# Kernel optimization log

Measured on AMD Instinct MI355X. Metric: run time of the kernel, lower is better.

## Reference

```python
import jax, jax.numpy as jnp
import numpy as np

CLIP_MIN = 0.0
CLIP_MAX = 1.0
B, T, F, E, CD = 64, 48, 128, 64, 32


def setup_inputs() -> dict:
    key = jax.random.key(0)
    ks = jax.random.split(key, 8)
    return {
        "input_x": jax.random.uniform(ks[0], (B, T, F), dtype=jnp.float32),
        "mask": jax.random.randint(ks[1], (B, T, F), 0, 2, dtype=jnp.int32),
        "embed0": jax.random.normal(ks[2], (F, E), dtype=jnp.float32) * 0.1,
        "embed1": jax.random.normal(ks[3], (F, E), dtype=jnp.float32) * 0.1,
        "embed_missing": jax.random.normal(ks[4], (F, E), dtype=jnp.float32) * 0.1,
        "attention_f_w": jax.random.normal(ks[5], (F, E), dtype=jnp.float32) * 0.1,
        "attention_f_b": jnp.zeros((F,), dtype=jnp.float32),
        "compress_w": jax.random.normal(ks[6], (2 * E, CD), dtype=jnp.float32) * 0.1,
    }


def reference(input_x, mask, embed0, embed1, embed_missing, attention_f_w, attention_f_b, compress_w):
    b, t, f = input_x.shape
    # new_mask: feature observed anywhere in time -> [b, 1, f, 1] (broadcasts over time)
    m = (jnp.sum(mask, axis=-2) != 0).astype(input_x.dtype)[:, None, :, None]
    x = input_x[..., None]  # [b, t, f, 1]
    # interval embedding c: [b, t, f, e]
    c0 = (x - m * CLIP_MIN) * embed0
    c1 = (m * CLIP_MAX - x) * embed1
    c = (c0 + c1) / (CLIP_MAX - CLIP_MIN) + (1.0 - m) * embed_missing
    # pairwise scores: sum_e c_i * c_j * w_i + b_i  (avoids [b,t,f,f,e] materialization)
    scores = jnp.einsum("btie,btje->btij", c * attention_f_w, c) + attention_f_b[:, None]
    scores = jnp.clip(scores, -5.0, 5.0)
    off_diag = 1.0 - jnp.eye(f, dtype=c.dtype)
    masked_exps = jnp.exp(scores) * off_diag
    attn = masked_exps / (jnp.sum(masked_exps, axis=-1, keepdims=True) + 1e-8)  # [b,t,f,f]
    # weighted aggregation: sum_j attn_ij * (c_i * c_j) = c_i * (attn @ c)_i
    agg = c * jnp.einsum("btij,btje->btie", attn, c)
    a = jax.nn.relu(jnp.concatenate([c, agg], axis=-1))  # [b,t,f,2e]
    out = jnp.einsum("btfk,kd->btfd", a, compress_w)
    return out.reshape(b, t, f * compress_w.shape[-1])
```

## Files before the change

### kernel.cpp

```cpp
#include <hip/hip_runtime.h>

#define NB 64
#define NT 48
#define NF 128
#define NE 64
#define NCD 32

#define LOG2E 1.4426950408889634f

typedef __attribute__((ext_vector_type(8))) short bf16x8;
typedef __attribute__((ext_vector_type(4))) float f32x4;
typedef __attribute__((ext_vector_type(2))) uint u32x2;

#define WS_MFLAG 0
#define WS_DB    32768
#define WS_E1B   49152
#define WS_EMB   65536
#define WS_WLB   81920
#define WS_WT    98304
#define WS_BL    106496

__device__ __forceinline__ ushort f2bf(float x) {
    union { float f; uint u; } v; v.f = x;
    uint r = v.u + 0x7fffu + ((v.u >> 16) & 1u);
    return (ushort)(r >> 16);
}
__device__ __forceinline__ uint pk_bf16(float lo, float hi) {
    uint r; asm("v_cvt_pk_bf16_f32 %0, %1, %2" : "=v"(r) : "v"(lo), "v"(hi)); return r;
}
__device__ __forceinline__ float bflo(uint u) { union { uint u; float f; } v; v.u = u << 16; return v.f; }
__device__ __forceinline__ float bfhi(uint u) { union { uint u; float f; } v; v.u = u & 0xffff0000u; return v.f; }

#define TRR(dst, addr, IMM) \
    asm volatile("ds_read_b64_tr_b16 %0, %1 offset:" IMM : "=v"(dst) : "v"(addr))
#define PLSWAP(a, b) asm("v_permlane32_swap_b32 %0, %1" : "+v"(a), "+v"(b))

#define AGG_ISSUE(CR, TB, O0, O1, O2, O3, O4, O5, O6, O7) \
    TRR(CR[0], TB, O0); TRR(CR[1], TB, O1); \
    TRR(CR[2], TB, O2); TRR(CR[3], TB, O3); \
    TRR(CR[4], TB, O4); TRR(CR[5], TB, O5); \
    TRR(CR[6], TB, O6); TRR(CR[7], TB, O7);

#define AGG_CONSUME(CR, PF, AG) { \
    union { u32x2 d[2]; bf16x8 v; } q0, q1, q2, q3; \
    q0.d[0] = CR[0]; q0.d[1] = CR[1]; q1.d[0] = CR[2]; q1.d[1] = CR[3]; \
    q2.d[0] = CR[4]; q2.d[1] = CR[5]; q3.d[0] = CR[6]; q3.d[1] = CR[7]; \
    AG[0] = __builtin_amdgcn_mfma_f32_16x16x32_bf16(q0.v, PF, AG[0], 0, 0, 0); \
    AG[1] = __builtin_amdgcn_mfma_f32_16x16x32_bf16(q1.v, PF, AG[1], 0, 0, 0); \
    AG[2] = __builtin_amdgcn_mfma_f32_16x16x32_bf16(q2.v, PF, AG[2], 0, 0, 0); \
    AG[3] = __builtin_amdgcn_mfma_f32_16x16x32_bf16(q3.v, PF, AG[3], 0, 0, 0); }

#define PF_BUILD(PF, PP, KS) { \
    uint X0 = PP[4*(KS)], X1 = PP[4*(KS)+1], X2 = PP[4*(KS)+2], X3 = PP[4*(KS)+3]; \
    PLSWAP(X0, X2); PLSWAP(X1, X3); \
    PF.u[0] = X0; PF.u[1] = X1; PF.u[2] = X2; PF.u[3] = X3; }

#define LGKM_WAIT(N) \
    asm volatile("s_waitcnt lgkmcnt(" #N ")" ::: "memory"); \
    __builtin_amdgcn_sched_barrier(0);

__global__ __launch_bounds__(256) void prep_kernel(
    const int* __restrict__ mask, const float* __restrict__ e0, const float* __restrict__ e1,
    const float* __restrict__ em, const float* __restrict__ aw, const float* __restrict__ ab,
    const float* __restrict__ cw,
    uint* __restrict__ mflag, ushort* __restrict__ db, ushort* __restrict__ e1b,
    ushort* __restrict__ emb, ushort* __restrict__ wlb, ushort* __restrict__ wt,
    float* __restrict__ bl)
{
    const int blk = blockIdx.x, tid = threadIdx.x;
    if (blk < 32) {
        int idx = blk * 256 + tid;
        float e1v = e1[idx];
        e1b[idx] = f2bf(e1v);
        emb[idx] = f2bf(em[idx]);
        db[idx]  = f2bf(e0[idx] - e1v);
        wlb[idx] = f2bf(aw[idx] * LOG2E);
    } else if (blk < 64) {
        int idx = (blk - 32) * 256 + tid;
        int b = idx >> 7, f = idx & 127;
        const int* p = mask + b * (NT * NF) + f;
        int s = 0;
#pragma unroll
        for (int t = 0; t < NT; ++t) s += p[t * NF];
        mflag[idx] = (s != 0) ? 1u : 0u;
    } else if (blk < 80) {
        int idx = (blk - 64) * 256 + tid;
        int k = idx >> 5, d = idx & 31;
        int kd;
        if (k < 64) kd = k;
        else {
            int kk = k - 64;
            kd = 64 + ((kk & 51) | ((kk & 4) << 1) | ((kk & 8) >> 1));
        }
        wt[d * 128 + kd] = f2bf(cw[idx]);
    } else {
        if (tid < NF) bl[tid] = ab[tid] * LOG2E;
    }
}

__global__ __launch_bounds__(512, 4) void fused_kernel(
    const float* __restrict__ input_x, const uint* __restrict__ mflag,
    const ushort* __restrict__ db, const ushort* __restrict__ e1b, const ushort* __restrict__ emb,
    const ushort* __restrict__ wlb, const float* __restrict__ blog,
    const ushort* __restrict__ wt, float* __restrict__ out)
{
    __shared__ ushort sC[2 * 9248];

    const int tid = threadIdx.x;
    const int blk = blockIdx.x;
    const int b   = blk / 24;
    const int bt0 = b * NT + (blk % 24) * 2;
    const int bt1 = bt0 + 1;

    const int wv = tid >> 6, ln = tid & 63;
    const int lr = ln & 15, lg = ln >> 4;
    const int i0 = wv << 4, irow = i0 + lr;

    const float bl = blog[irow];
    const float x0 = input_x[bt0 * NF + irow];
    const float x1 = input_x[bt1 * NF + irow];
    const ushort* Mrow = (mflag[b * NF + irow] ? e1b : emb) + irow * NE;
    const ushort* Drow = db + irow * NE;
    const ushort* Wrow = wlb + irow * NE;

    const int sbase = (lg >> 1) * 2312 + (lr >> 2) * 72 + (lr & 3) * 16 + (lg & 1) * 8;

    ushort* sC0 = sC;
    ushort* sC1 = sC + 9248;

    bf16x8 cwf0[2], cwf1[2];
#pragma unroll
    for (int ks = 0; ks < 2; ++ks) {
        const int eo = ks * 32 + lg * 8;
        uint d4[4], m4[4], w4[4];
        *(uint4*)d4 = *(const uint4*)(Drow + eo);
        *(uint4*)m4 = *(const uint4*)(Mrow + eo);
        *(uint4*)w4 = *(const uint4*)(Wrow + eo);
        uint cb0[4], cb1[4];
        union { uint u[4]; bf16x8 v; } cw0, cw1;
#pragma unroll
        for (int j = 0; j < 4; ++j) {
            float dlo = bflo(d4[j]), dhi = bfhi(d4[j]);
            float mlo = bflo(m4[j]), mhi = bfhi(m4[j]);
            float wlo = bflo(w4[j]), whi = bfhi(w4[j]);
            float c0lo = fmaf(x0, dlo, mlo), c0hi = fmaf(x0, dhi, mhi);
            float c1lo = fmaf(x1, dlo, mlo), c1hi = fmaf(x1, dhi, mhi);
            cb0[j] = pk_bf16(c0lo, c0hi);
            cb1[j] = pk_bf16(c1lo, c1hi);
            cw0.u[j] = pk_bf16(c0lo * wlo, c0hi * whi);
            cw1.u[j] = pk_bf16(c1lo * wlo, c1hi * whi);
        }
        cwf0[ks] = cw0.v; cwf1[ks] = cw1.v;
        *(uint4*)&sC0[sbase + wv * 288 + ks * 4624] = *(uint4*)cb0;
        *(uint4*)&sC1[sbase + wv * 288 + ks * 4624] = *(uint4*)cb1;
    }
    __syncthreads();

    auto run_S4 = [&](const ushort* base, bf16x8 w0, bf16x8 w1, int jt0, f32x4* st4) {
#pragma unroll
        for (int j = 0; j < 4; ++j) {
            const int jt = jt0 + j;
            f32x4 a = (f32x4){bl, bl, bl, bl};
            bf16x8 a0 = *(bf16x8*)&base[sbase + jt * 288];
            a = __builtin_amdgcn_mfma_f32_16x16x32_bf16(a0, w0, a, 0, 0, 0);
            bf16x8 a1 = *(bf16x8*)&base[sbase + jt * 288 + 4624];
            a = __builtin_amdgcn_mfma_f32_16x16x32_bf16(a1, w1, a, 0, 0, 0);
            st4[j] = a;
        }
    };
    auto run_SM4 = [&](f32x4* st4, uint* pp, int jt0, float* rsa) {
#pragma unroll
        for (int j = 0; j < 4; ++j) {
            const int jt = jt0 + j;
            f32x4 v = st4[j];
            float e0 = exp2f(v[0]);
            float e1 = exp2f(v[1]);
            float e2 = exp2f(v[2]);
            float e3 = exp2f(v[3]);
            if (jt == wv) {
                const bool on = (lg == (lr >> 2));
                e0 = (on && (lr & 3) == 0) ? 0.f : e0;
                e1 = (on && (lr & 3) == 1) ? 0.f : e1;
                e2 = (on && (lr & 3) == 2) ? 0.f : e2;
                e3 = (on && (lr & 3) == 3) ? 0.f : e3;
            }
            rsa[0] += e0; rsa[1] += e1; rsa[2] += e2; rsa[3] += e3;
            pp[2 * jt]     = pk_bf16(e0, e1);
            pp[2 * jt + 1] = pk_bf16(e2, e3);
        }
    };
    auto run_chainS = [&](const ushort* base, bf16x8 w0, bf16x8 w1, uint* pp) -> float {
        f32x4 st4[4];
        float rsa[4] = {0.f, 0.f, 0.f, 0.f};
        run_S4(base, w0, w1, 0, st4);
        run_SM4(st4, pp, 0, rsa);
        run_S4(base, w0, w1, 4, st4);
        run_SM4(st4, pp, 4, rsa);
        float rs = (rsa[0] + rsa[1]) + (rsa[2] + rsa[3]);
        rs += __shfl_xor(rs, 16);
        rs += __shfl_xor(rs, 32);
        return 1.0f / (rs + 1e-8f);
    };
    auto run_AGG = [&](const ushort* base, uint* pp, f32x4* ag) {
#pragma unroll
        for (int et = 0; et < 4; ++et) ag[et] = (f32x4){0.f, 0.f, 0.f, 0.f};
        const uint tb = (uint)(uintptr_t)base
                      + 2u * (uint)(72 * (((lg >> 1) << 2) + (lg & 1)) + lr);
        u32x2 cA[8], cB[8];
        union { uint u[4]; bf16x8 v; } pf0, pf1, pf2, pf3;
        PF_BUILD(pf0, pp, 0);
        AGG_ISSUE(cA, tb, "0", "144", "4624", "4768", "9248", "9392", "13872", "14016");
        PF_BUILD(pf1, pp, 1);
        AGG_ISSUE(cB, tb, "1152", "1296", "5776", "5920", "10400", "10544", "15024", "15168");
        LGKM_WAIT(8);
        AGG_CONSUME(cA, pf0.v, ag);
        PF_BUILD(pf2, pp, 2);
        AGG_ISSUE(cA, tb, "2304", "2448", "6928", "7072", "11552", "11696", "16176", "16320");
        LGKM_WAIT(8);
        AGG_CONSUME(cB, pf1.v, ag);
        PF_BUILD(pf3, pp, 3);
        AGG_ISSUE(cB, tb, "3456", "3600", "8080", "8224", "12704", "12848", "17328", "17472");
        LGKM_WAIT(8);
        AGG_CONSUME(cA, pf2.v, ag);
        LGKM_WAIT(0);
        AGG_CONSUME(cB, pf3.v, ag);
    };
    auto run_EPI = [&](const ushort* base, f32x4* ag, float inv, uint* aa) {
        const int ebase = (wv * 4 + (lr >> 2)) * 72 + (lr & 3) * 16 + lg * 4;
#pragma unroll
        for (int et = 0; et < 4; ++et) {
            u32x2 cb2 = *(u32x2*)&base[ebase + et * 2312];
            float a0f = fmaxf(ag[et][0] * inv * bflo(cb2.x), 0.f);
            float a1f = fmaxf(ag[et][1] * inv * bfhi(cb2.x), 0.f);
            float a2f = fmaxf(ag[et][2] * inv * bflo(cb2.y), 0.f);
            float a3f = fmaxf(ag[et][3] * inv * bfhi(cb2.y), 0.f);
            aa[2 * et]     = pk_bf16(a0f, a1f);
            aa[2 * et + 1] = pk_bf16(a2f, a3f);
        }
    };
    auto run_OUT = [&](const ushort* base, uint* aa, const bf16x8* wf, int bt) {
        f32x4 oc[2];
        oc[0] = (f32x4){0.f, 0.f, 0.f, 0.f};
        oc[1] = (f32x4){0.f, 0.f, 0.f, 0.f};
#pragma unroll
        for (int ks = 0; ks < 4; ++ks) {
            bf16x8 afr;
            if (ks < 2) {
                const uint4 cc = *(uint4*)&base[sbase + wv * 288 + ks * 4624];
                union { uint u[4]; bf16x8 v; } rl;
                asm("v_pk_max_i16 %0, %1, 0" : "=v"(rl.u[0]) : "v"(cc.x));
                asm("v_pk_max_i16 %0, %1, 0" : "=v"(rl.u[1]) : "v"(cc.y));
                asm("v_pk_max_i16 %0, %1, 0" : "=v"(rl.u[2]) : "v"(cc.z));
                asm("v_pk_max_i16 %0, %1, 0" : "=v"(rl.u[3]) : "v"(cc.w));
                afr = rl.v;
            } else {
                const int kk = ks - 2;
                uint Y0 = aa[4 * kk], Y1 = aa[4 * kk + 1], Y2 = aa[4 * kk + 2], Y3 = aa[4 * kk + 3];
                PLSWAP(Y0, Y2);
                PLSWAP(Y1, Y3);
                union { uint u[4]; bf16x8 v; } af;
                af.u[0] = Y0; af.u[1] = Y1; af.u[2] = Y2; af.u[3] = Y3;
                afr = af.v;
            }
            oc[0] = __builtin_amdgcn_mfma_f32_16x16x32_bf16(afr, wf[ks * 2 + 0], oc[0], 0, 0, 0);
            oc[1] = __builtin_amdgcn_mfma_f32_16x16x32_bf16(afr, wf[ks * 2 + 1], oc[1], 0, 0, 0);
        }
        float* op = out + bt * (NF * NCD);
#pragma unroll
        for (int dt = 0; dt < 2; ++dt)
#pragma unroll
            for (int r = 0; r < 4; ++r)
                op[(i0 + lg * 4 + r) * NCD + dt * 16 + lr] = oc[dt][r];
    };

    uint pp0[16], pp1[16];
    f32x4 ag0[4], ag1[4];
    uint aa0[8], aa1[8];

    const float inv0 = run_chainS(sC0, cwf0[0], cwf0[1], pp0);
    const float inv1 = run_chainS(sC1, cwf1[0], cwf1[1], pp1);

    run_AGG(sC0, pp0, ag0);
    run_EPI(sC0, ag0, inv0, aa0);
    run_AGG(sC1, pp1, ag1);

    bf16x8 wf[8];
#pragma unroll
    for (int ks = 0; ks < 4; ++ks)
#pragma unroll
        for (int dt = 0; dt < 2; ++dt)
            wf[ks * 2 + dt] = *(const bf16x8*)(wt + (dt * 16 + lr) * 128 + ks * 32 + lg * 8);

    run_EPI(sC1, ag1, inv1, aa1);
    run_OUT(sC0, aa0, wf, bt0);
    run_OUT(sC1, aa1, wf, bt1);
}

extern "C" void kernel_launch(void* const* d_in, const int* in_sizes, int n_in,
                              void* d_out, int out_size, void* d_ws, size_t ws_size,
                              hipStream_t stream) {
    const float* input_x       = (const float*)d_in[0];
    const int*   mask          = (const int*)d_in[1];
    const float* embed0        = (const float*)d_in[2];
    const float* embed1        = (const float*)d_in[3];
    const float* embed_missing = (const float*)d_in[4];
    const float* attn_w        = (const float*)d_in[5];
    const float* attn_b        = (const float*)d_in[6];
    const float* compress_w    = (const float*)d_in[7];
    float* out = (float*)d_out;

    char* ws = (char*)d_ws;
    uint*   mflag = (uint*)(ws + WS_MFLAG);
    ushort* dbp   = (ushort*)(ws + WS_DB);
    ushort* e1bp  = (ushort*)(ws + WS_E1B);
    ushort* embp  = (ushort*)(ws + WS_EMB);
    ushort* wlbp  = (ushort*)(ws + WS_WLB);
    ushort* wtp   = (ushort*)(ws + WS_WT);
    float*  blp   = (float*)(ws + WS_BL);

    hipLaunchKernelGGL(prep_kernel, dim3(81), dim3(256), 0, stream,
                       mask, embed0, embed1, embed_missing, attn_w, attn_b, compress_w,
                       mflag, dbp, e1bp, embp, wlbp, wtp, blp);
    hipLaunchKernelGGL(fused_kernel, dim3(NB * NT / 2), dim3(512), 0, stream,
                       input_x, mflag, dbp, e1bp, embp, wlbp, blp, wtp, out);
}
```

Baseline: 41.94 us.

## Process one (b,t) per block with each wave owning two row tiles

Changes the work split from two (b,t) slices per 512-thread block to one slice per 256-thread block, with each of 4 waves handling 32 rows (two 16-row groups). The aggregation step reuses each transposed LDS read of c for two MFMAs (one per row group), halving LDS traffic per MFMA. Shared memory per block halves and the grid doubles. The trade-off is higher register pressure per wave (two sets of P fragments and accumulators) under launch bounds of 256 threads with a minimum of 3 blocks.

```diff
diff --git a/kernel.cpp b/kernel.cpp
--- a/kernel.cpp
+++ b/kernel.cpp
@@ -41,14 +41,18 @@
     TRR(CR[4], TB, O4); TRR(CR[5], TB, O5); \
     TRR(CR[6], TB, O6); TRR(CR[7], TB, O7);
 
-#define AGG_CONSUME(CR, PF, AG) { \
+#define AGG_CONSUME2(CR, PFA, PFB, AGA, AGB) { \
     union { u32x2 d[2]; bf16x8 v; } q0, q1, q2, q3; \
     q0.d[0] = CR[0]; q0.d[1] = CR[1]; q1.d[0] = CR[2]; q1.d[1] = CR[3]; \
     q2.d[0] = CR[4]; q2.d[1] = CR[5]; q3.d[0] = CR[6]; q3.d[1] = CR[7]; \
-    AG[0] = __builtin_amdgcn_mfma_f32_16x16x32_bf16(q0.v, PF, AG[0], 0, 0, 0); \
-    AG[1] = __builtin_amdgcn_mfma_f32_16x16x32_bf16(q1.v, PF, AG[1], 0, 0, 0); \
-    AG[2] = __builtin_amdgcn_mfma_f32_16x16x32_bf16(q2.v, PF, AG[2], 0, 0, 0); \
-    AG[3] = __builtin_amdgcn_mfma_f32_16x16x32_bf16(q3.v, PF, AG[3], 0, 0, 0); }
+    AGA[0] = __builtin_amdgcn_mfma_f32_16x16x32_bf16(q0.v, PFA, AGA[0], 0, 0, 0); \
+    AGB[0] = __builtin_amdgcn_mfma_f32_16x16x32_bf16(q0.v, PFB, AGB[0], 0, 0, 0); \
+    AGA[1] = __builtin_amdgcn_mfma_f32_16x16x32_bf16(q1.v, PFA, AGA[1], 0, 0, 0); \
+    AGB[1] = __builtin_amdgcn_mfma_f32_16x16x32_bf16(q1.v, PFB, AGB[1], 0, 0, 0); \
+    AGA[2] = __builtin_amdgcn_mfma_f32_16x16x32_bf16(q2.v, PFA, AGA[2], 0, 0, 0); \
+    AGB[2] = __builtin_amdgcn_mfma_f32_16x16x32_bf16(q2.v, PFB, AGB[2], 0, 0, 0); \
+    AGA[3] = __builtin_amdgcn_mfma_f32_16x16x32_bf16(q3.v, PFA, AGA[3], 0, 0, 0); \
+    AGB[3] = __builtin_amdgcn_mfma_f32_16x16x32_bf16(q3.v, PFB, AGB[3], 0, 0, 0); }
 
 #define PF_BUILD(PF, PP, KS) { \
     uint X0 = PP[4*(KS)], X1 = PP[4*(KS)+1], X2 = PP[4*(KS)+2], X3 = PP[4*(KS)+3]; \
@@ -98,138 +102,143 @@
     }
 }
 
-__global__ __launch_bounds__(512, 4) void fused_kernel(
+__global__ __launch_bounds__(256, 3) void fused_kernel(
     const float* __restrict__ input_x, const uint* __restrict__ mflag,
     const ushort* __restrict__ db, const ushort* __restrict__ e1b, const ushort* __restrict__ emb,
     const ushort* __restrict__ wlb, const float* __restrict__ blog,
     const ushort* __restrict__ wt, float* __restrict__ out)
 {
-    __shared__ ushort sC[2 * 9248];
+    __shared__ ushort sC[9248];
 
     const int tid = threadIdx.x;
-    const int blk = blockIdx.x;
-    const int b   = blk / 24;
-    const int bt0 = b * NT + (blk % 24) * 2;
-    const int bt1 = bt0 + 1;
+    const int bt = blockIdx.x;
+    const int b = bt / NT;
 
     const int wv = tid >> 6, ln = tid & 63;
     const int lr = ln & 15, lg = ln >> 4;
-    const int i0 = wv << 4, irow = i0 + lr;
-
-    const float bl = blog[irow];
-    const float x0 = input_x[bt0 * NF + irow];
-    const float x1 = input_x[bt1 * NF + irow];
-    const ushort* Mrow = (mflag[b * NF + irow] ? e1b : emb) + irow * NE;
-    const ushort* Drow = db + irow * NE;
-    const ushort* Wrow = wlb + irow * NE;
-
-    const int sbase = (lg >> 1) * 2312 + (lr >> 2) * 72 + (lr & 3) * 16 + (lg & 1) * 8;
-
-    ushort* sC0 = sC;
-    ushort* sC1 = sC + 9248;
-
-    bf16x8 cwf0[2], cwf1[2];
-#pragma unroll
-    for (int ks = 0; ks < 2; ++ks) {
-        const int eo = ks * 32 + lg * 8;
-        uint d4[4], m4[4], w4[4];
-        *(uint4*)d4 = *(const uint4*)(Drow + eo);
-        *(uint4*)m4 = *(const uint4*)(Mrow + eo);
-        *(uint4*)w4 = *(const uint4*)(Wrow + eo);
-        uint cb0[4], cb1[4];
-        union { uint u[4]; bf16x8 v; } cw0, cw1;
-#pragma unroll
-        for (int j = 0; j < 4; ++j) {
-            float dlo = bflo(d4[j]), dhi = bfhi(d4[j]);
-            float mlo = bflo(m4[j]), mhi = bfhi(m4[j]);
-            float wlo = bflo(w4[j]), whi = bfhi(w4[j]);
-            float c0lo = fmaf(x0, dlo, mlo), c0hi = fmaf(x0, dhi, mhi);
-            float c1lo = fmaf(x1, dlo, mlo), c1hi = fmaf(x1, dhi, mhi);
-            cb0[j] = pk_bf16(c0lo, c0hi);
-            cb1[j] = pk_bf16(c1lo, c1hi);
-            cw0.u[j] = pk_bf16(c0lo * wlo, c0hi * whi);
-            cw1.u[j] = pk_bf16(c1lo * wlo, c1hi * whi);
-        }
-        cwf0[ks] = cw0.v; cwf1[ks] = cw1.v;
-        *(uint4*)&sC0[sbase + wv * 288 + ks * 4624] = *(uint4*)cb0;
-        *(uint4*)&sC1[sbase + wv * 288 + ks * 4624] = *(uint4*)cb1;
+    const int irow0 = wv * 32 + lr;
+
+    const int abase = (lg >> 1) * 2312 + (lr >> 2) * 72 + (lr & 3) * 16 + (lg & 1) * 8;
+
+    const float bl0 = blog[irow0];
+    const float bl1 = blog[irow0 + 16];
+
+    bf16x8 cwf[2][2];
+#pragma unroll
+    for (int g = 0; g < 2; ++g) {
+        const int irow = irow0 + g * 16;
+        const float x = input_x[bt * NF + irow];
+        const ushort* Mrow = (mflag[b * NF + irow] ? e1b : emb) + irow * NE;
+        const ushort* Drow = db + irow * NE;
+        const ushort* Wrow = wlb + irow * NE;
+#pragma unroll
+        for (int ks = 0; ks < 2; ++ks) {
+            const int eo = ks * 32 + lg * 8;
+            uint d4[4], m4[4], w4[4];
+            *(uint4*)d4 = *(const uint4*)(Drow + eo);
+            *(uint4*)m4 = *(const uint4*)(Mrow + eo);
+            *(uint4*)w4 = *(const uint4*)(Wrow + eo);
+            uint cb[4]; union { uint u[4]; bf16x8 v; } cu;
+#pragma unroll
+            for (int j = 0; j < 4; ++j) {
+                float clo = fmaf(x, bflo(d4[j]), bflo(m4[j]));
+                float chi = fmaf(x, bfhi(d4[j]), bfhi(m4[j]));
+                cb[j] = pk_bf16(clo, chi);
+                cu.u[j] = pk_bf16(clo * bflo(w4[j]), chi * bfhi(w4[j]));
+            }
+            cwf[g][ks] = cu.v;
+            *(uint4*)&sC[abase + (wv * 2 + g) * 288 + ks * 4624] = *(uint4*)cb;
+        }
     }
     __syncthreads();
 
-    auto run_S4 = [&](const ushort* base, bf16x8 w0, bf16x8 w1, int jt0, f32x4* st4) {
-#pragma unroll
-        for (int j = 0; j < 4; ++j) {
-            const int jt = jt0 + j;
-            f32x4 a = (f32x4){bl, bl, bl, bl};
-            bf16x8 a0 = *(bf16x8*)&base[sbase + jt * 288];
-            a = __builtin_amdgcn_mfma_f32_16x16x32_bf16(a0, w0, a, 0, 0, 0);
-            bf16x8 a1 = *(bf16x8*)&base[sbase + jt * 288 + 4624];
-            a = __builtin_amdgcn_mfma_f32_16x16x32_bf16(a1, w1, a, 0, 0, 0);
-            st4[j] = a;
-        }
-    };
-    auto run_SM4 = [&](f32x4* st4, uint* pp, int jt0, float* rsa) {
-#pragma unroll
-        for (int j = 0; j < 4; ++j) {
-            const int jt = jt0 + j;
-            f32x4 v = st4[j];
-            float e0 = exp2f(v[0]);
-            float e1 = exp2f(v[1]);
-            float e2 = exp2f(v[2]);
-            float e3 = exp2f(v[3]);
-            if (jt == wv) {
-                const bool on = (lg == (lr >> 2));
-                e0 = (on && (lr & 3) == 0) ? 0.f : e0;
-                e1 = (on && (lr & 3) == 1) ? 0.f : e1;
-                e2 = (on && (lr & 3) == 2) ? 0.f : e2;
-                e3 = (on && (lr & 3) == 3) ? 0.f : e3;
+    uint pp0[16], pp1[16];
+    float inv0, inv1;
+    {
+        f32x4 st[8];
+#pragma unroll
+        for (int g = 0; g < 2; ++g) {
+            const float blv = g ? bl1 : bl0;
+            uint* pp = g ? pp1 : pp0;
+#pragma unroll
+            for (int jt = 0; jt < 8; ++jt) {
+                f32x4 a = (f32x4){blv, blv, blv, blv};
+                bf16x8 a0 = *(bf16x8*)&sC[abase + jt * 288];
+                a = __builtin_amdgcn_mfma_f32_16x16x32_bf16(a0, cwf[g][0], a, 0, 0, 0);
+                bf16x8 a1 = *(bf16x8*)&sC[abase + jt * 288 + 4624];
+                a = __builtin_amdgcn_mfma_f32_16x16x32_bf16(a1, cwf[g][1], a, 0, 0, 0);
+                st[jt] = a;
             }
-            rsa[0] += e0; rsa[1] += e1; rsa[2] += e2; rsa[3] += e3;
-            pp[2 * jt]     = pk_bf16(e0, e1);
-            pp[2 * jt + 1] = pk_bf16(e2, e3);
-        }
-    };
-    auto run_chainS = [&](const ushort* base, bf16x8 w0, bf16x8 w1, uint* pp) -> float {
-        f32x4 st4[4];
-        float rsa[4] = {0.f, 0.f, 0.f, 0.f};
-        run_S4(base, w0, w1, 0, st4);
-        run_SM4(st4, pp, 0, rsa);
-        run_S4(base, w0, w1, 4, st4);
-        run_SM4(st4, pp, 4, rsa);
-        float rs = (rsa[0] + rsa[1]) + (rsa[2] + rsa[3]);
-        rs += __shfl_xor(rs, 16);
-        rs += __shfl_xor(rs, 32);
-        return 1.0f / (rs + 1e-8f);
-    };
-    auto run_AGG = [&](const ushort* base, uint* pp, f32x4* ag) {
-#pragma unroll
-        for (int et = 0; et < 4; ++et) ag[et] = (f32x4){0.f, 0.f, 0.f, 0.f};
-        const uint tb = (uint)(uintptr_t)base
+            const int dt_ = wv * 2 + g;
+            float rs0 = 0.f, rs1 = 0.f, rs2 = 0.f, rs3 = 0.f;
+#pragma unroll
+            for (int jt = 0; jt < 8; ++jt) {
+                f32x4 v = st[jt];
+                float e0 = exp2f(v[0]);
+                float e1 = exp2f(v[1]);
+                float e2 = exp2f(v[2]);
+                float e3 = exp2f(v[3]);
+                if (jt == dt_) {
+                    const bool on = (lg == (lr >> 2));
+                    e0 = (on && (lr & 3) == 0) ? 0.f : e0;
+                    e1 = (on && (lr & 3) == 1) ? 0.f : e1;
+                    e2 = (on && (lr & 3) == 2) ? 0.f : e2;
+                    e3 = (on && (lr & 3) == 3) ? 0.f : e3;
+                }
+                rs0 += e0; rs1 += e1; rs2 += e2; rs3 += e3;
+                pp[2 * jt]     = pk_bf16(e0, e1);
+                pp[2 * jt + 1] = pk_bf16(e2, e3);
+            }
+            float rs = (rs0 + rs1) + (rs2 + rs3);
+            rs += __shfl_xor(rs, 16);
+            rs += __shfl_xor(rs, 32);
+            if (g) inv1 = 1.0f / (rs + 1e-8f); else inv0 = 1.0f / (rs + 1e-8f);
+        }
+    }
+
+    f32x4 agA[4], agB[4];
+#pragma unroll
+    for (int et = 0; et < 4; ++et) { agA[et] = (f32x4){0.f,0.f,0.f,0.f}; agB[et] = (f32x4){0.f,0.f,0.f,0.f}; }
+    {
+        const uint tb = (uint)(uintptr_t)&sC[0]
                       + 2u * (uint)(72 * (((lg >> 1) << 2) + (lg & 1)) + lr);
         u32x2 cA[8], cB[8];
-        union { uint u[4]; bf16x8 v; } pf0, pf1, pf2, pf3;
-        PF_BUILD(pf0, pp, 0);
+        union { uint u[4]; bf16x8 v; } pfA0, pfB0, pfA1, pfB1, pfA2, pfB2, pfA3, pfB3;
+        PF_BUILD(pfA0, pp0, 0); PF_BUILD(pfB0, pp1, 0);
         AGG_ISSUE(cA, tb, "0", "144", "4624", "4768", "9248", "9392", "13872", "14016");
-        PF_BUILD(pf1, pp, 1);
+        PF_BUILD(pfA1, pp0, 1); PF_BUILD(pfB1, pp1, 1);
         AGG_ISSUE(cB, tb, "1152", "1296", "5776", "5920", "10400", "10544", "15024", "15168");
         LGKM_WAIT(8);
-        AGG_CONSUME(cA, pf0.v, ag);
-        PF_BUILD(pf2, pp, 2);
+        AGG_CONSUME2(cA, pfA0.v, pfB0.v, agA, agB);
+        PF_BUILD(pfA2, pp0, 2); PF_BUILD(pfB2, pp1, 2);
         AGG_ISSUE(cA, tb, "2304", "2448", "6928", "7072", "11552", "11696", "16176", "16320");
         LGKM_WAIT(8);
-        AGG_CONSUME(cB, pf1.v, ag);
-        PF_BUILD(pf3, pp, 3);
+        AGG_CONSUME2(cB, pfA1.v, pfB1.v, agA, agB);
+        PF_BUILD(pfA3, pp0, 3); PF_BUILD(pfB3, pp1, 3);
         AGG_ISSUE(cB, tb, "3456", "3600", "8080", "8224", "12704", "12848", "17328", "17472");
         LGKM_WAIT(8);
-        AGG_CONSUME(cA, pf2.v, ag);
+        AGG_CONSUME2(cA, pfA2.v, pfB2.v, agA, agB);
         LGKM_WAIT(0);
-        AGG_CONSUME(cB, pf3.v, ag);
-    };
-    auto run_EPI = [&](const ushort* base, f32x4* ag, float inv, uint* aa) {
-        const int ebase = (wv * 4 + (lr >> 2)) * 72 + (lr & 3) * 16 + lg * 4;
+        AGG_CONSUME2(cB, pfA3.v, pfB3.v, agA, agB);
+    }
+
+    bf16x8 wf[8];
+#pragma unroll
+    for (int ks = 0; ks < 4; ++ks)
+#pragma unroll
+        for (int dt = 0; dt < 2; ++dt)
+            wf[ks * 2 + dt] = *(const bf16x8*)(wt + (dt * 16 + lr) * 128 + ks * 32 + lg * 8);
+
+    uint aa0[8], aa1[8];
+#pragma unroll
+    for (int g = 0; g < 2; ++g) {
+        const f32x4* ag = g ? agB : agA;
+        const float inv = g ? inv1 : inv0;
+        uint* aa = g ? aa1 : aa0;
+        const int ebase = (wv * 8 + g * 4 + (lr >> 2)) * 72 + (lr & 3) * 16 + lg * 4;
 #pragma unroll
         for (int et = 0; et < 4; ++et) {
-            u32x2 cb2 = *(u32x2*)&base[ebase + et * 2312];
+            u32x2 cb2 = *(u32x2*)&sC[ebase + et * 2312];
             float a0f = fmaxf(ag[et][0] * inv * bflo(cb2.x), 0.f);
             float a1f = fmaxf(ag[et][1] * inv * bfhi(cb2.x), 0.f);
             float a2f = fmaxf(ag[et][2] * inv * bflo(cb2.y), 0.f);
@@ -237,8 +246,12 @@
             aa[2 * et]     = pk_bf16(a0f, a1f);
             aa[2 * et + 1] = pk_bf16(a2f, a3f);
         }
-    };
-    auto run_OUT = [&](const ushort* base, uint* aa, const bf16x8* wf, int bt) {
+    }
+
+    float* op = out + bt * (NF * NCD);
+#pragma unroll
+    for (int g = 0; g < 2; ++g) {
+        uint* aa = g ? aa1 : aa0;
         f32x4 oc[2];
         oc[0] = (f32x4){0.f, 0.f, 0.f, 0.f};
         oc[1] = (f32x4){0.f, 0.f, 0.f, 0.f};
@@ -246,7 +259,7 @@
         for (int ks = 0; ks < 4; ++ks) {
             bf16x8 afr;
             if (ks < 2) {
-                const uint4 cc = *(uint4*)&base[sbase + wv * 288 + ks * 4624];
+                const uint4 cc = *(uint4*)&sC[abase + (wv * 2 + g) * 288 + ks * 4624];
                 union { uint u[4]; bf16x8 v; } rl;
                 asm("v_pk_max_i16 %0, %1, 0" : "=v"(rl.u[0]) : "v"(cc.x));
                 asm("v_pk_max_i16 %0, %1, 0" : "=v"(rl.u[1]) : "v"(cc.y));
@@ -265,35 +278,12 @@
             oc[0] = __builtin_amdgcn_mfma_f32_16x16x32_bf16(afr, wf[ks * 2 + 0], oc[0], 0, 0, 0);
             oc[1] = __builtin_amdgcn_mfma_f32_16x16x32_bf16(afr, wf[ks * 2 + 1], oc[1], 0, 0, 0);
         }
-        float* op = out + bt * (NF * NCD);
 #pragma unroll
         for (int dt = 0; dt < 2; ++dt)
 #pragma unroll
             for (int r = 0; r < 4; ++r)
-                op[(i0 + lg * 4 + r) * NCD + dt * 16 + lr] = oc[dt][r];
-    };
-
-    uint pp0[16], pp1[16];
-    f32x4 ag0[4], ag1[4];
-    uint aa0[8], aa1[8];
-
-    const float inv0 = run_chainS(sC0, cwf0[0], cwf0[1], pp0);
-    const float inv1 = run_chainS(sC1, cwf1[0], cwf1[1], pp1);
-
-    run_AGG(sC0, pp0, ag0);
-    run_EPI(sC0, ag0, inv0, aa0);
-    run_AGG(sC1, pp1, ag1);
-
-    bf16x8 wf[8];
-#pragma unroll
-    for (int ks = 0; ks < 4; ++ks)
-#pragma unroll
-        for (int dt = 0; dt < 2; ++dt)
-            wf[ks * 2 + dt] = *(const bf16x8*)(wt + (dt * 16 + lr) * 128 + ks * 32 + lg * 8);
-
-    run_EPI(sC1, ag1, inv1, aa1);
-    run_OUT(sC0, aa0, wf, bt0);
-    run_OUT(sC1, aa1, wf, bt1);
+                op[(wv * 32 + g * 16 + lg * 4 + r) * NCD + dt * 16 + lr] = oc[dt][r];
+    }
 }
 
 extern "C" void kernel_launch(void* const* d_in, const int* in_sizes, int n_in,
@@ -321,6 +311,6 @@
     hipLaunchKernelGGL(prep_kernel, dim3(81), dim3(256), 0, stream,
                        mask, embed0, embed1, embed_missing, attn_w, attn_b, compress_w,
                        mflag, dbp, e1bp, embp, wlbp, wtp, blp);
-    hipLaunchKernelGGL(fused_kernel, dim3(NB * NT / 2), dim3(512), 0, stream,
+    hipLaunchKernelGGL(fused_kernel, dim3(NB * NT), dim3(256), 0, stream,
                        input_x, mflag, dbp, e1bp, embp, wlbp, blp, wtp, out);
 }
```

After: 44.76 us. 6.7% more time.
